# Performance work log

Hardware: AMD Instinct MI355X
Metric: run time of the kernel (lower is better)

The kernel has to match this reference:

```python
import jax, jax.numpy as jnp
import numpy as np

W, H = 512, 512
SHIFT_NORM = 100.0
P = 1
WEIGHT = 10.0
EPS = 1e-16


def _cv_matrix(angle, scale, shift, cx, cy):
    # cv2.getRotationMatrix2D-style matrix (pixel coords) with extra x-shift.
    alpha = scale * jnp.cos(angle)
    beta = scale * jnp.sin(angle)
    row0 = jnp.stack([alpha, beta, (1.0 - alpha) * cx - beta * cy + shift], axis=-1)
    row1 = jnp.stack([-beta, alpha, beta * cx + (1.0 - alpha) * cy], axis=-1)
    return jnp.stack([row0, row1], axis=-2)  # [B,2,3]


def _normalize_transform(M, width, height):
    # Convert pixel-space affine to normalized [-1,1] coords (align_corners=True).
    a, b, tx = M[:, 0, 0], M[:, 0, 1], M[:, 0, 2]
    c, d, ty = M[:, 1, 0], M[:, 1, 1], M[:, 1, 2]
    sw = float(width - 1)
    sh = float(height - 1)
    A = a
    Bc = b * sh / sw
    Cc = a + b * sh / sw + 2.0 * tx / sw - 1.0
    D = c * sw / sh
    E = d
    Fc = c * sw / sh + d + 2.0 * ty / sh - 1.0
    row0 = jnp.stack([A, Bc, Cc], axis=-1)
    row1 = jnp.stack([D, E, Fc], axis=-1)
    return jnp.stack([row0, row1], axis=-2)  # [B,2,3]


def _affine_grid(T, height, width):
    # torch affine_grid, align_corners=True
    u = jnp.linspace(-1.0, 1.0, width, dtype=T.dtype)
    v = jnp.linspace(-1.0, 1.0, height, dtype=T.dtype)
    vv, uu = jnp.meshgrid(v, u, indexing='ij')
    base = jnp.stack([uu, vv, jnp.ones_like(uu)], axis=-1)  # [H,W,3]
    return jnp.einsum('bij,hwj->bhwi', T, base)  # [B,H,W,2] (x,y)


def _grid_sample(img, grid):
    # bilinear, zeros padding, align_corners=True. img [B,C,H,W], grid [B,Ho,Wo,2]
    B, C, Hi, Wi = img.shape
    x = (grid[..., 0] + 1.0) * (Wi - 1) / 2.0
    y = (grid[..., 1] + 1.0) * (Hi - 1) / 2.0
    x0 = jnp.floor(x)
    y0 = jnp.floor(y)
    wx1 = x - x0
    wy1 = y - y0
    wx0 = 1.0 - wx1
    wy0 = 1.0 - wy1

    def gather(xi, yi):
        valid = ((xi >= 0) & (xi < Wi) & (yi >= 0) & (yi < Hi)).astype(img.dtype)
        xc = jnp.clip(xi, 0, Wi - 1).astype(jnp.int32)
        yc = jnp.clip(yi, 0, Hi - 1).astype(jnp.int32)
        g = jax.vmap(lambda im, xb, yb, vb: im[:, yb, xb] * vb[None])
        return g(img, xc, yc, valid)  # [B,C,Ho,Wo]

    out = (gather(x0, y0) * (wx0 * wy0)[:, None]
           + gather(x0 + 1, y0) * (wx1 * wy0)[:, None]
           + gather(x0, y0 + 1) * (wx0 * wy1)[:, None]
           + gather(x0 + 1, y0 + 1) * (wx1 * wy1)[:, None])
    return out


def setup_inputs() -> dict:
    key = jax.random.key(0)
    k1, k2, k3 = jax.random.split(key, 3)
    theta = jax.random.normal(k1, (32, 3), dtype=jnp.float32)
    img_R = jax.random.normal(k2, (32, 3, H, W), dtype=jnp.float32)
    img_R_orig = jax.random.normal(k3, (32, 3, H, W), dtype=jnp.float32)
    return {"theta": theta, "img_R": img_R, "img_R_orig": img_R_orig}


def reference(theta, img_R, img_R_orig):
    cx, cy = W // 2, H // 2
    M = _cv_matrix(theta[:, 0], theta[:, 1], SHIFT_NORM * theta[:, 2], cx, cy)
    T = _normalize_transform(M, W, H)
    grid = _affine_grid(T, H, W)
    warped = _grid_sample(img_R_orig, grid)
    mask = jnp.ones((img_R.shape[0], 1, H, W), dtype=img_R.dtype)
    warped_mask = _grid_sample(mask, grid)[:, 0]  # [B,H,W]
    # p=1 norm over channel dim
    nrm = jnp.sum(jnp.abs(img_R - warped), axis=1)  # [B,H,W]
    num = jnp.sum(warped_mask * nrm, axis=(1, 2)) + EPS
    den = jnp.sum(warped_mask, axis=(1, 2)) + EPS
    losses = WEIGHT * num / den
    return jnp.mean(losses)
```

## Files before the change

### kernel.cpp

```cpp
#include <hip/hip_runtime.h>
#include <math.h>

#define IMG_W 512
#define IMG_H 512
#define NB 32
#define NC 3
#define PLANE (IMG_H * IMG_W)

#define TILE_W 32
#define TILE_H 32
#define TILES_X (IMG_W / TILE_W)
#define TILES_Y (IMG_H / TILE_H)
#define TILES_PER_B (TILES_X * TILES_Y)
#define NBLOCKS (NB * TILES_PER_B)

typedef float vfloat4 __attribute__((ext_vector_type(4)));


__global__ __launch_bounds__(256) void recon_main(
    const float* __restrict__ theta,
    const float* __restrict__ img_R,
    const float* __restrict__ img_orig,
    float* __restrict__ ws)
{
    const int lin = blockIdx.x;
    const int xcd = lin & 7;
    const int loc = lin >> 3;
    const int b   = xcd * 4 + (loc >> 8);
    const int tile = loc & 255;
    const int tx = (tile & (TILES_X - 1)) * TILE_W;
    const int ty = (tile >> 4) * TILE_H;

    const int tid  = threadIdx.x;
    const int trow = tid >> 3;
    const int tcol = (tid & 7) * 4;

    const float ang   = theta[b * 3 + 0];
    const float s     = theta[b * 3 + 1];
    const float shift = 100.0f * theta[b * 3 + 2];
    float sn, cs;
    sincosf(ang, &sn, &cs);
    const float alpha = s * cs;
    const float beta  = s * sn;
    const float tx_a = (1.0f - alpha) * 256.0f - beta * 256.0f + shift;
    const float ty_a = beta * 256.0f + (1.0f - alpha) * 256.0f;
    const float Cc = alpha + beta + 2.0f * tx_a / 511.0f - 1.0f;
    const float Fc = -beta + alpha + 2.0f * ty_a / 511.0f - 1.0f;
    const float X0 = 255.5f * (Cc + 1.0f - alpha - beta);
    const float Y0 = 255.5f * (Fc + 1.0f + beta - alpha);

    const float* orig_b = img_orig + (size_t)b * NC * PLANE;
    const float* R_b    = img_R    + (size_t)b * NC * PLANE;

    const int h  = ty + trow;
    const int w0 = tx + tcol;
    const int p0 = h * IMG_W + w0;

    const float xb = X0 + alpha * (float)w0 + beta * (float)h;
    const float yb = Y0 - beta * (float)w0 + alpha * (float)h;

    int   a0[4], a1[4], sl0[4], sl1[4];
    float w00[4], w10[4], w01[4], w11[4], mk[4];
    float den_acc = 0.0f;

#pragma unroll
    for (int j = 0; j < 4; ++j) {
        const float x = xb + alpha * (float)j;
        const float y = yb - beta  * (float)j;
        const float x0f = floorf(x), y0f = floorf(y);
        const float fx1 = x - x0f,  fy1 = y - y0f;
        const float fx0 = 1.0f - fx1, fy0 = 1.0f - fy1;
        const float vx0 = (x0f >=  0.0f && x0f <= 511.0f) ? 1.0f : 0.0f;
        const float vx1 = (x0f >= -1.0f && x0f <= 510.0f) ? 1.0f : 0.0f;
        const float vy0 = (y0f >=  0.0f && y0f <= 511.0f) ? 1.0f : 0.0f;
        const float vy1 = (y0f >= -1.0f && y0f <= 510.0f) ? 1.0f : 0.0f;
        const int xi0 = (int)fminf(fmaxf(x0f,        0.0f), 511.0f);
        const int xi1 = (int)fminf(fmaxf(x0f + 1.0f, 0.0f), 511.0f);
        const int yi0 = (int)fminf(fmaxf(y0f,        0.0f), 511.0f);
        const int yi1 = (int)fminf(fmaxf(y0f + 1.0f, 0.0f), 511.0f);
        const int xc  = min(xi0, 510);
        w00[j] = fx0 * fy0 * vx0 * vy0;
        w10[j] = fx1 * fy0 * vx1 * vy0;
        w01[j] = fx0 * fy1 * vx0 * vy1;
        w11[j] = fx1 * fy1 * vx1 * vy1;
        mk[j]  = w00[j] + w10[j] + w01[j] + w11[j];
        a0[j]  = yi0 * IMG_W + xc;
        a1[j]  = yi1 * IMG_W + xc;
        sl0[j] = xi0 - xc;
        sl1[j] = xi1 - xc;
        den_acc += mk[j];
    }

    float nrm[4] = {0.0f, 0.0f, 0.0f, 0.0f};
#pragma unroll
    for (int c = 0; c < NC; ++c) {
        const float* plane = orig_b + c * PLANE;
        const vfloat4 rv = __builtin_nontemporal_load(
                             (const vfloat4*)(R_b + c * PLANE + p0));
        const float rj[4] = {rv.x, rv.y, rv.z, rv.w};
#pragma unroll
        for (int j = 0; j < 4; ++j) {
            const float2 t0 = *(const float2*)(plane + a0[j]);
            const float2 t1 = *(const float2*)(plane + a1[j]);
            const float s00 = sl0[j] ? t0.y : t0.x;
            const float s10 = sl1[j] ? t0.y : t0.x;
            const float s01 = sl0[j] ? t1.y : t1.x;
            const float s11 = sl1[j] ? t1.y : t1.x;
            const float warped = s00 * w00[j] + s10 * w10[j]
                               + s01 * w01[j] + s11 * w11[j];
            nrm[j] += fabsf(rj[j] - warped);
        }
    }
    float num_acc = 0.0f;
#pragma unroll
    for (int j = 0; j < 4; ++j) num_acc += mk[j] * nrm[j];

#pragma unroll
    for (int off = 32; off > 0; off >>= 1) {
        num_acc += __shfl_down(num_acc, off);
        den_acc += __shfl_down(den_acc, off);
    }

    __shared__ float snum[4];
    __shared__ float sden[4];
    const int wave = threadIdx.x >> 6;
    const int lane = threadIdx.x & 63;
    if (lane == 0) { snum[wave] = num_acc; sden[wave] = den_acc; }
    __syncthreads();
    if (threadIdx.x == 0) {
        ws[lin]           = snum[0] + snum[1] + snum[2] + snum[3];
        ws[NBLOCKS + lin] = sden[0] + sden[1] + sden[2] + sden[3];
    }
}

__global__ __launch_bounds__(256) void recon_final(
    const float* __restrict__ ws,
    float* __restrict__ out)
{
    __shared__ float sloss[NB];
    const int t = threadIdx.x;
    const int b = t >> 3;
    const int j = t & 7;

    float n = 0.0f, d = 0.0f;
    for (int k = 0; k < 32; ++k) {
        const int tile = j * 32 + k;
        const int lin  = ((b & 3) * 256 + tile) * 8 + (b >> 2);
        n += ws[lin];
        d += ws[NBLOCKS + lin];
    }
#pragma unroll
    for (int off = 4; off > 0; off >>= 1) {
        n += __shfl_down(n, off);
        d += __shfl_down(d, off);
    }
    if (j == 0) sloss[b] = 10.0f * (n + 1e-16f) / (d + 1e-16f);
    __syncthreads();
    if (t == 0) {
        float L = 0.0f;
#pragma unroll
        for (int i = 0; i < NB; ++i) L += sloss[i];
        out[0] = L * (1.0f / (float)NB);
    }
}

extern "C" void kernel_launch(void* const* d_in, const int* in_sizes, int n_in,
                              void* d_out, int out_size, void* d_ws, size_t ws_size,
                              hipStream_t stream) {
    const float* theta    = (const float*)d_in[0];
    const float* img_R    = (const float*)d_in[1];
    const float* img_orig = (const float*)d_in[2];
    float* out = (float*)d_out;
    float* ws  = (float*)d_ws;

    recon_main<<<NBLOCKS, 256, 0, stream>>>(theta, img_R, img_orig, ws);
    recon_final<<<1, 256, 0, stream>>>(ws, out);
}
```

Measured before the change: 258.5 us.

## Stage warped source bounding box into LDS before bilinear gathers

Each block computes the bounding box of the source region its output tile maps to, cooperatively loads that box per channel into shared memory with vectorized coalesced loads, then does the four bilinear taps from LDS. A fallback keeps the old global-gather path when the box exceeds the LDS budget or 128 columns. This aims to replace scattered global gathers with coalesced loads and LDS reads, at the cost of 24KB LDS per block (lower occupancy), extra barriers per channel, and loading unused box area for rotated tiles.

```diff
diff --git a/kernel.cpp b/kernel.cpp
--- a/kernel.cpp
+++ b/kernel.cpp
@@ -14,6 +14,8 @@
 #define TILES_PER_B (TILES_X * TILES_Y)
 #define NBLOCKS (NB * TILES_PER_B)
 
+#define LDSF 6144
+
 typedef float vfloat4 __attribute__((ext_vector_type(4)));
 
 
@@ -23,6 +25,10 @@
     const float* __restrict__ img_orig,
     float* __restrict__ ws)
 {
+    __shared__ __align__(16) float tileLds[LDSF];
+    __shared__ float snum[4];
+    __shared__ float sden[4];
+
     const int lin = blockIdx.x;
     const int xcd = lin & 7;
     const int loc = lin >> 3;
@@ -59,7 +65,7 @@
     const float xb = X0 + alpha * (float)w0 + beta * (float)h;
     const float yb = Y0 - beta * (float)w0 + alpha * (float)h;
 
-    int   a0[4], a1[4], sl0[4], sl1[4];
+    int   xi0a[4], xi1a[4], yi0a[4], yi1a[4];
     float w00[4], w10[4], w01[4], w11[4], mk[4];
     float den_acc = 0.0f;
 
@@ -74,43 +80,123 @@
         const float vx1 = (x0f >= -1.0f && x0f <= 510.0f) ? 1.0f : 0.0f;
         const float vy0 = (y0f >=  0.0f && y0f <= 511.0f) ? 1.0f : 0.0f;
         const float vy1 = (y0f >= -1.0f && y0f <= 510.0f) ? 1.0f : 0.0f;
-        const int xi0 = (int)fminf(fmaxf(x0f,        0.0f), 511.0f);
-        const int xi1 = (int)fminf(fmaxf(x0f + 1.0f, 0.0f), 511.0f);
-        const int yi0 = (int)fminf(fmaxf(y0f,        0.0f), 511.0f);
-        const int yi1 = (int)fminf(fmaxf(y0f + 1.0f, 0.0f), 511.0f);
-        const int xc  = min(xi0, 510);
+        xi0a[j] = (int)fminf(fmaxf(x0f,        0.0f), 511.0f);
+        xi1a[j] = (int)fminf(fmaxf(x0f + 1.0f, 0.0f), 511.0f);
+        yi0a[j] = (int)fminf(fmaxf(y0f,        0.0f), 511.0f);
+        yi1a[j] = (int)fminf(fmaxf(y0f + 1.0f, 0.0f), 511.0f);
         w00[j] = fx0 * fy0 * vx0 * vy0;
         w10[j] = fx1 * fy0 * vx1 * vy0;
         w01[j] = fx0 * fy1 * vx0 * vy1;
         w11[j] = fx1 * fy1 * vx1 * vy1;
         mk[j]  = w00[j] + w10[j] + w01[j] + w11[j];
-        a0[j]  = yi0 * IMG_W + xc;
-        a1[j]  = yi1 * IMG_W + xc;
-        sl0[j] = xi0 - xc;
-        sl1[j] = xi1 - xc;
         den_acc += mk[j];
     }
 
+    const float fx_lo = (float)tx, fx_hi = (float)(tx + TILE_W - 1);
+    const float fy_lo = (float)ty, fy_hi = (float)(ty + TILE_H - 1);
+    const float cxA = X0 + alpha * fx_lo + beta * fy_lo;
+    const float cxB = X0 + alpha * fx_hi + beta * fy_lo;
+    const float cxC = X0 + alpha * fx_lo + beta * fy_hi;
+    const float cxD = X0 + alpha * fx_hi + beta * fy_hi;
+    const float cyA = Y0 - beta * fx_lo + alpha * fy_lo;
+    const float cyB = Y0 - beta * fx_hi + alpha * fy_lo;
+    const float cyC = Y0 - beta * fx_lo + alpha * fy_hi;
+    const float cyD = Y0 - beta * fx_hi + alpha * fy_hi;
+    const float min_x = fminf(fminf(cxA, cxB), fminf(cxC, cxD));
+    const float max_x = fmaxf(fmaxf(cxA, cxB), fmaxf(cxC, cxD));
+    const float min_y = fminf(fminf(cyA, cyB), fminf(cyC, cyD));
+    const float max_y = fmaxf(fmaxf(cyA, cyB), fmaxf(cyC, cyD));
+
+    int xlo = (int)floorf(min_x);
+    int xhi = (int)floorf(max_x) + 1;
+    xlo = min(max(xlo, 0), 511);
+    xhi = min(max(xhi, 0), 511);
+    xlo &= ~3;
+    int ylo = (int)floorf(min_y);
+    int yhi = (int)floorf(max_y) + 1;
+    ylo = min(max(ylo, 0), 511);
+    yhi = min(max(yhi, 0), 511);
+
+    const int bw = xhi - xlo + 1;
+    const int bh = yhi - ylo + 1;
+    int stride = (bw + 3) & ~3;
+    if (((stride >> 2) & 1) == 0) stride += 4;
+    const int nq4 = stride >> 2;
+    const bool staged = (stride * bh <= LDSF) && (nq4 <= 32);
+
     float nrm[4] = {0.0f, 0.0f, 0.0f, 0.0f};
-#pragma unroll
-    for (int c = 0; c < NC; ++c) {
-        const float* plane = orig_b + c * PLANE;
-        const vfloat4 rv = __builtin_nontemporal_load(
-                             (const vfloat4*)(R_b + c * PLANE + p0));
-        const float rj[4] = {rv.x, rv.y, rv.z, rv.w};
+
+    if (staged) {
+        int l00[4], l10[4], l01[4], l11[4];
 #pragma unroll
         for (int j = 0; j < 4; ++j) {
-            const float2 t0 = *(const float2*)(plane + a0[j]);
-            const float2 t1 = *(const float2*)(plane + a1[j]);
-            const float s00 = sl0[j] ? t0.y : t0.x;
-            const float s10 = sl1[j] ? t0.y : t0.x;
-            const float s01 = sl0[j] ? t1.y : t1.x;
-            const float s11 = sl1[j] ? t1.y : t1.x;
-            const float warped = s00 * w00[j] + s10 * w10[j]
-                               + s01 * w01[j] + s11 * w11[j];
-            nrm[j] += fabsf(rj[j] - warped);
-        }
-    }
+            const int r0 = (yi0a[j] - ylo) * stride - xlo;
+            const int r1 = (yi1a[j] - ylo) * stride - xlo;
+            l00[j] = r0 + xi0a[j];
+            l10[j] = r0 + xi1a[j];
+            l01[j] = r1 + xi0a[j];
+            l11[j] = r1 + xi1a[j];
+        }
+        const int qq  = tid & 31;
+        const int r00 = tid >> 5;
+        const int col = xlo + (qq << 2);
+        const bool doload = (col <= xhi);
+
+        for (int c = 0; c < NC; ++c) {
+            if (c) __syncthreads();
+            const float* plane = orig_b + c * PLANE;
+            if (doload) {
+                for (int r = r00; r < bh; r += 8) {
+                    const vfloat4 v = *(const vfloat4*)(plane + (ylo + r) * IMG_W + col);
+                    *(vfloat4*)(&tileLds[r * stride + (qq << 2)]) = v;
+                }
+            }
+            __syncthreads();
+            const vfloat4 rv = __builtin_nontemporal_load(
+                                 (const vfloat4*)(R_b + c * PLANE + p0));
+            const float rj[4] = {rv.x, rv.y, rv.z, rv.w};
+#pragma unroll
+            for (int j = 0; j < 4; ++j) {
+                const float s00 = tileLds[l00[j]];
+                const float s10 = tileLds[l10[j]];
+                const float s01 = tileLds[l01[j]];
+                const float s11 = tileLds[l11[j]];
+                const float warped = s00 * w00[j] + s10 * w10[j]
+                                   + s01 * w01[j] + s11 * w11[j];
+                nrm[j] += fabsf(rj[j] - warped);
+            }
+        }
+    } else {
+        int a0[4], a1[4], sl0[4], sl1[4];
+#pragma unroll
+        for (int j = 0; j < 4; ++j) {
+            const int xc = min(xi0a[j], 510);
+            a0[j]  = yi0a[j] * IMG_W + xc;
+            a1[j]  = yi1a[j] * IMG_W + xc;
+            sl0[j] = xi0a[j] - xc;
+            sl1[j] = xi1a[j] - xc;
+        }
+#pragma unroll
+        for (int c = 0; c < NC; ++c) {
+            const float* plane = orig_b + c * PLANE;
+            const vfloat4 rv = __builtin_nontemporal_load(
+                                 (const vfloat4*)(R_b + c * PLANE + p0));
+            const float rj[4] = {rv.x, rv.y, rv.z, rv.w};
+#pragma unroll
+            for (int j = 0; j < 4; ++j) {
+                const float2 t0 = *(const float2*)(plane + a0[j]);
+                const float2 t1 = *(const float2*)(plane + a1[j]);
+                const float s00 = sl0[j] ? t0.y : t0.x;
+                const float s10 = sl1[j] ? t0.y : t0.x;
+                const float s01 = sl0[j] ? t1.y : t1.x;
+                const float s11 = sl1[j] ? t1.y : t1.x;
+                const float warped = s00 * w00[j] + s10 * w10[j]
+                                   + s01 * w01[j] + s11 * w11[j];
+                nrm[j] += fabsf(rj[j] - warped);
+            }
+        }
+    }
+
     float num_acc = 0.0f;
 #pragma unroll
     for (int j = 0; j < 4; ++j) num_acc += mk[j] * nrm[j];
@@ -121,8 +207,6 @@
         den_acc += __shfl_down(den_acc, off);
     }
 
-    __shared__ float snum[4];
-    __shared__ float sden[4];
     const int wave = threadIdx.x >> 6;
     const int lane = threadIdx.x & 63;
     if (lane == 0) { snum[wave] = num_acc; sden[wave] = den_acc; }
```

Measured after the change: 253.0 us. 2.2% less time.
